# Optimization experiments

Measured on AMD Instinct MI355X. Metric: run time of the kernel, lower is better.

Reference implementation:

```python
import jax, jax.numpy as jnp
import numpy as np

DIM = 1024
HEADS = 16
DIM_HEAD = 64
INNER = HEADS * DIM_HEAD  # 1024
B, N = 2, 2048


def setup_inputs() -> dict:
    key = jax.random.key(0)
    ks = jax.random.split(key, 8)
    q = jax.random.normal(ks[0], (B, N, DIM), dtype=jnp.float32)
    k = jax.random.normal(ks[1], (B, N, DIM), dtype=jnp.float32)
    v = jax.random.normal(ks[2], (B, N, DIM), dtype=jnp.float32)
    # True = masked out (masked_fill semantics); causal mask broadcast over batch
    causal = jnp.triu(jnp.ones((N, N), dtype=jnp.bool_), k=1)
    mask = jnp.broadcast_to(causal, (B, N, N))
    s = 0.02
    Wq = jax.random.normal(ks[3], (DIM, INNER), dtype=jnp.float32) * s
    Wk = jax.random.normal(ks[4], (DIM, INNER), dtype=jnp.float32) * s
    Wv = jax.random.normal(ks[5], (DIM, INNER), dtype=jnp.float32) * s
    Wo = jax.random.normal(ks[6], (INNER, DIM), dtype=jnp.float32) * s
    bo = jnp.zeros((DIM,), dtype=jnp.float32)
    return {"q": q, "k": k, "v": v, "mask": mask,
            "Wq": Wq, "Wk": Wk, "Wv": Wv, "Wo": Wo, "bo": bo}


def reference(q, k, v, mask, Wq, Wk, Wv, Wo, bo):
    h, d = HEADS, DIM_HEAD
    scale = d ** -0.5
    b, n, _ = q.shape

    def heads_split(x):  # [b, n, h*d] -> [b, h, n, d]
        return x.reshape(b, -1, h, d).transpose(0, 2, 1, 3)

    qh = heads_split(q @ Wq)
    kh = heads_split(k @ Wk)
    vh = heads_split(v @ Wv)

    dots = jnp.einsum('bhid,bhjd->bhij', qh, kh) * scale  # [b,h,n,n]
    mask_value = -jnp.finfo(dots.dtype).max
    dots = jnp.where(mask[:, None, :, :], mask_value, dots)
    attn = jax.nn.softmax(dots, axis=-1)
    out = jnp.einsum('bhij,bhjd->bhid', attn, vh)          # [b,h,n,d]
    out = out.transpose(0, 2, 1, 3).reshape(b, n, h * d)    # [b,n,h*d]
    out = out @ Wo + bo                                     # RowParallelLinear (bias=True)
    return out  # dropout p=0.0 is identity
```

## Files before the change

### kernel.cpp

```cpp
#include <hip/hip_runtime.h>

typedef __attribute__((ext_vector_type(8))) short short8;
typedef __attribute__((ext_vector_type(4))) float f32x4;
typedef __attribute__((ext_vector_type(4))) unsigned int u32x4;

#define MFMA_BF16(a, b, c) __builtin_amdgcn_mfma_f32_16x16x32_bf16((a), (b), (c), 0, 0, 0)

#define GLOAD16(g, l) __builtin_amdgcn_global_load_lds( \
    (const __attribute__((address_space(1))) void*)(g),  \
    (__attribute__((address_space(3))) void*)(l), 16, 0, 0)

#define BARRIER() __builtin_amdgcn_s_barrier()
#define LGKMCNT0() do { asm volatile("s_waitcnt lgkmcnt(0)" ::: "memory"); \
                        __builtin_amdgcn_sched_barrier(0); } while (0)
#define VMCNT(n) asm volatile("s_waitcnt vmcnt(" n ")" ::: "memory")

static __device__ __forceinline__ unsigned short f2bf(float f) {
    unsigned int u = __builtin_bit_cast(unsigned int, f);
    u += 0x7fffu + ((u >> 16) & 1u);
    return (unsigned short)(u >> 16);
}
static __device__ __forceinline__ unsigned int cvtpk(float a, float b) {
    unsigned int r;
    asm("v_cvt_pk_bf16_f32 %0, %1, %2" : "=v"(r) : "v"(a), "v"(b));
    return r;
}
static __device__ __forceinline__ float ex2(float x) {
    float r;
    asm("v_exp_f32 %0, %1" : "=v"(r) : "v"(x));
    return r;
}

__global__ __launch_bounds__(256) void convX_kernel(
    const float* __restrict__ q, const float* __restrict__ k, const float* __restrict__ v,
    unsigned short* __restrict__ dq, unsigned short* __restrict__ dk,
    unsigned short* __restrict__ dv)
{
    const float* s; unsigned short* d;
    switch (blockIdx.y) {
        case 0:  s = q; d = dq; break;
        case 1:  s = k; d = dk; break;
        default: s = v; d = dv; break;
    }
    int i = (blockIdx.x * 256 + threadIdx.x) * 8;
    float4 a = *reinterpret_cast<const float4*>(s + i);
    float4 b = *reinterpret_cast<const float4*>(s + i + 4);
    short8 o;
    o[0] = (short)f2bf(a.x); o[1] = (short)f2bf(a.y);
    o[2] = (short)f2bf(a.z); o[3] = (short)f2bf(a.w);
    o[4] = (short)f2bf(b.x); o[5] = (short)f2bf(b.y);
    o[6] = (short)f2bf(b.z); o[7] = (short)f2bf(b.w);
    *reinterpret_cast<short8*>(d + i) = o;
}

__global__ __launch_bounds__(256) void convWT_kernel(
    const float* __restrict__ w0, const float* __restrict__ w1,
    const float* __restrict__ w2, const float* __restrict__ w3,
    unsigned short* __restrict__ t0, unsigned short* __restrict__ t1,
    unsigned short* __restrict__ t2, unsigned short* __restrict__ t3)
{
    const float* W; unsigned short* T;
    switch (blockIdx.z) {
        case 0:  W = w0; T = t0; break;
        case 1:  W = w1; T = t1; break;
        case 2:  W = w2; T = t2; break;
        default: W = w3; T = t3; break;
    }
    __shared__ unsigned short ldsT[64][72];
    const int t = threadIdx.x;
    const int kb = blockIdx.x * 64, cb = blockIdx.y * 64;

    const int c4 = (t & 15) * 4;
    const int r0 = t >> 4;
    #pragma unroll
    for (int i = 0; i < 4; ++i) {
        int kr = r0 + i * 16;
        float4 wv = *reinterpret_cast<const float4*>(&W[(size_t)(kb + kr) * 1024 + cb + c4]);
        ldsT[c4 + 0][kr] = f2bf(wv.x);
        ldsT[c4 + 1][kr] = f2bf(wv.y);
        ldsT[c4 + 2][kr] = f2bf(wv.z);
        ldsT[c4 + 3][kr] = f2bf(wv.w);
    }
    __syncthreads();
    const int c = t >> 2;
    const int kp = (t & 3) * 16;
    short8 o0 = *reinterpret_cast<const short8*>(&ldsT[c][kp]);
    short8 o1 = *reinterpret_cast<const short8*>(&ldsT[c][kp + 8]);
    *reinterpret_cast<short8*>(&T[(size_t)(cb + c) * 1024 + kb + kp])     = o0;
    *reinterpret_cast<short8*>(&T[(size_t)(cb + c) * 1024 + kb + kp + 8]) = o1;
}

__global__ __launch_bounds__(512, 2) void qkv_gemm(
    const unsigned short* __restrict__ Xq, const unsigned short* __restrict__ Xk,
    const unsigned short* __restrict__ Xv,
    const unsigned short* __restrict__ WqT, const unsigned short* __restrict__ WkT,
    const unsigned short* __restrict__ WvT,
    unsigned short* __restrict__ Qh, unsigned short* __restrict__ Kh,
    unsigned short* __restrict__ VhT)
{
    extern __shared__ unsigned short lds[];
    const int t    = threadIdx.x;
    const int lane = t & 63, w = t >> 6;
    const int lr   = lane & 15, lg = lane >> 4;
    const int wrow = w >> 2, wcol = w & 3;
    const int sw   = lr & 7;

    const int z = blockIdx.z;
    const unsigned short *A, *B; unsigned short* dst;
    int tm, cn;
    if (z == 2)      { A = WvT; B = Xv;  dst = VhT; tm = blockIdx.y * 256; cn = blockIdx.x * 256; }
    else if (z == 1) { A = Xk;  B = WkT; dst = Kh;  tm = blockIdx.x * 256; cn = blockIdx.y * 256; }
    else             { A = Xq;  B = WqT; dst = Qh;  tm = blockIdx.x * 256; cn = blockIdx.y * 256; }

    const unsigned short* Ag = A + (size_t)tm * 1024;
    const unsigned short* Bg = B + (size_t)cn * 1024;

    const int sr    = t >> 3;
    const int gsw   = (t & 7) ^ (sr & 7);
    const int brow0 = (sr >> 5) * 64 + (sr & 31);

    auto stageA = [&](int q, int kt, unsigned short* slabA) {
        const unsigned short* g = Ag + (size_t)(q * 64 + sr) * 1024 + kt + gsw * 8;
        GLOAD16(g, slabA + q * 8192 + t * 8);
        GLOAD16(g + (size_t)128 * 1024, slabA + q * 8192 + 4096 + t * 8);
    };
    auto stageB = [&](int s, int kt, unsigned short* slabB) {
        const unsigned short* g = Bg + (size_t)(brow0 + s * 32) * 1024 + kt + gsw * 8;
        GLOAD16(g, slabB + s * 8192 + t * 8);
        GLOAD16(g + (size_t)128 * 1024, slabB + s * 8192 + 4096 + t * 8);
    };

    short8 rA[4][2], rB0[2][2], rB1[2][2];
    auto ldA = [&](const unsigned short* bufA, int q) {
        #pragma unroll
        for (int m2 = 0; m2 < 4; ++m2) {
            const unsigned short* p = bufA + q * 8192 + (wrow * 64 + m2 * 16 + lr) * 64;
            rA[m2][0] = *reinterpret_cast<const short8*>(p + (lg ^ sw) * 8);
            rA[m2][1] = *reinterpret_cast<const short8*>(p + ((4 + lg) ^ sw) * 8);
        }
    };
    auto ldB = [&](const unsigned short* bufB, int s, short8 rB[2][2]) {
        #pragma unroll
        for (int n2 = 0; n2 < 2; ++n2) {
            const unsigned short* p = bufB + s * 8192 + (wcol * 32 + n2 * 16 + lr) * 64;
            rB[n2][0] = *reinterpret_cast<const short8*>(p + (lg ^ sw) * 8);
            rB[n2][1] = *reinterpret_cast<const short8*>(p + ((4 + lg) ^ sw) * 8);
        }
    };

    f32x4 acc[8][4];
    #pragma unroll
    for (int i = 0; i < 8; ++i)
        #pragma unroll
        for (int j = 0; j < 4; ++j) acc[i][j] = (f32x4){0.f, 0.f, 0.f, 0.f};

#define QUAD(MH, NH, RB) do {                                            \
    _Pragma("unroll")                                                    \
    for (int m2 = 0; m2 < 4; ++m2) {                                     \
        _Pragma("unroll")                                                \
        for (int n2 = 0; n2 < 2; ++n2) {                                 \
            f32x4 c_ = acc[(MH)*4 + m2][(NH)*2 + n2];                    \
            c_ = MFMA_BF16(rA[m2][0], (RB)[n2][0], c_);                  \
            c_ = MFMA_BF16(rA[m2][1], (RB)[n2][1], c_);                  \
            acc[(MH)*4 + m2][(NH)*2 + n2] = c_;                          \
        } } } while (0)

    stageA(0, 0, lds);
    stageB(0, 0, lds + 16384);
    stageB(1, 0, lds + 16384);
    stageA(1, 0, lds);
    VMCNT("4");
    BARRIER();

    for (int tt = 0; tt < 15; ++tt) {
        unsigned short* cA = lds + (tt & 1) * 32768;
        unsigned short* cB = cA + 16384;
        unsigned short* nA = lds + ((tt + 1) & 1) * 32768;
        unsigned short* nB = nA + 16384;
        const int kn = (tt + 1) * 64;
        stageA(0, kn, nA);
        ldA(cA, 0); ldB(cB, 0, rB0);
        VMCNT("4"); BARRIER(); LGKMCNT0();
        __builtin_amdgcn_s_setprio(1); QUAD(0, 0, rB0); __builtin_amdgcn_s_setprio(0);
        BARRIER();
        stageB(0, kn, nB);
        ldB(cB, 1, rB1);
        VMCNT("4"); BARRIER(); LGKMCNT0();
        __builtin_amdgcn_s_setprio(1); QUAD(0, 1, rB1); __builtin_amdgcn_s_setprio(0);
        BARRIER();
        stageB(1, kn, nB);
        ldA(cA, 1);
        BARRIER(); LGKMCNT0();
        __builtin_amdgcn_s_setprio(1); QUAD(1, 1, rB1); __builtin_amdgcn_s_setprio(0);
        BARRIER();
        stageA(1, kn, nA);
        VMCNT("4"); BARRIER(); LGKMCNT0();
        __builtin_amdgcn_s_setprio(1); QUAD(1, 0, rB0); __builtin_amdgcn_s_setprio(0);
        BARRIER();
    }
    {
        unsigned short* cA = lds + 32768;
        unsigned short* cB = cA + 16384;
        ldA(cA, 0); ldB(cB, 0, rB0);
        VMCNT("2"); BARRIER(); LGKMCNT0();
        __builtin_amdgcn_s_setprio(1); QUAD(0, 0, rB0); __builtin_amdgcn_s_setprio(0);
        BARRIER();
        ldB(cB, 1, rB1);
        VMCNT("0"); BARRIER(); LGKMCNT0();
        __builtin_amdgcn_s_setprio(1); QUAD(0, 1, rB1); __builtin_amdgcn_s_setprio(0);
        BARRIER();
        ldA(cA, 1);
        LGKMCNT0();
        __builtin_amdgcn_s_setprio(1); QUAD(1, 1, rB1); QUAD(1, 0, rB0);
        __builtin_amdgcn_s_setprio(0);
    }
#undef QUAD

    if (z == 2) {
        #pragma unroll
        for (int mi = 0; mi < 8; ++mi)
            #pragma unroll
            for (int ni = 0; ni < 4; ++ni)
                #pragma unroll
                for (int r = 0; r < 4; ++r) {
                    int c    = tm + wrow * 128 + mi * 16 + lg * 4 + r;
                    int nseq = cn + wcol * 64 + ni * 16 + lr;
                    int b = nseq >> 11, n = nseq & 2047;
                    int h = c >> 6, d = c & 63;
                    dst[(((size_t)(b * 16 + h) * 64 + d) << 11) + n] = f2bf(acc[mi][ni][r]);
                }
    } else {
        const float sc = (z == 0) ? 0.18033688011112042f : 1.0f;
        #pragma unroll
        for (int mi = 0; mi < 8; ++mi)
            #pragma unroll
            for (int ni = 0; ni < 4; ++ni)
                #pragma unroll
                for (int r = 0; r < 4; ++r) {
                    int orow = tm + wrow * 128 + mi * 16 + lg * 4 + r;
                    int ocol = cn + wcol * 64 + ni * 16 + lr;
                    int b = orow >> 11, n = orow & 2047;
                    int h = ocol >> 6, d = ocol & 63;
                    dst[(((size_t)(b * 16 + h) * 2048 + n) << 6) + d] = f2bf(acc[mi][ni][r] * sc);
                }
    }
}

__global__ __launch_bounds__(256) void o_gemm(
    const unsigned short* __restrict__ Ctx, const unsigned short* __restrict__ WoT,
    const float* __restrict__ bias, float* __restrict__ out)
{
    __shared__ unsigned short LB[3][8192];
    const int t = threadIdx.x;
    const int lane = t & 63, w = t >> 6;
    const int lr = lane & 15, lg = lane >> 4;
    const int wr = w >> 1, wc = w & 1;
    const int tm = blockIdx.x * 128, cn = blockIdx.y * 128;

    const int srow = w * 16 + (lane >> 2);
    const int sk   = (lane & 3) * 8;
    const unsigned short* ga = Ctx + (size_t)(tm + srow) * 1024 + sk;
    const unsigned short* gb = WoT + (size_t)(cn + srow) * 1024 + sk;
    const int lo = srow * 32 + sk;

    auto stage = [&](int k0, int bf) {
        GLOAD16(ga + k0, &LB[bf][lo]);
        GLOAD16(ga + k0 + (size_t)64 * 1024, &LB[bf][64 * 32 + lo]);
        GLOAD16(gb + k0, &LB[bf][4096 + lo]);
        GLOAD16(gb + k0 + (size_t)64 * 1024, &LB[bf][4096 + 64 * 32 + lo]);
    };

    f32x4 acc[4][4];
    #pragma unroll
    for (int i = 0; i < 4; ++i)
        #pragma unroll
        for (int j = 0; j < 4; ++j) acc[i][j] = (f32x4){0.f, 0.f, 0.f, 0.f};

    stage(0, 0);
    stage(32, 1);

    int cur = 0;
    for (int s = 0; s < 32; ++s) {
        if (s + 1 < 32) { VMCNT("4"); } else { VMCNT("0"); }
        BARRIER();
        __builtin_amdgcn_sched_barrier(0);
        if (s + 2 < 32) {
            int nb = cur + 2; if (nb >= 3) nb -= 3;
            stage(32 * (s + 2), nb);
        }

        short8 af[4], bfr[4];
        #pragma unroll
        for (int i = 0; i < 4; ++i) {
            af[i]  = *reinterpret_cast<const short8*>(&LB[cur][(wr * 64 + i * 16 + lr) * 32 + lg * 8]);
            bfr[i] = *reinterpret_cast<const short8*>(&LB[cur][4096 + (wc * 64 + i * 16 + lr) * 32 + lg * 8]);
        }
        __builtin_amdgcn_s_setprio(1);
        #pragma unroll
        for (int mi = 0; mi < 4; ++mi)
            #pragma unroll
            for (int ni = 0; ni < 4; ++ni)
                acc[mi][ni] = MFMA_BF16(af[mi], bfr[ni], acc[mi][ni]);
        __builtin_amdgcn_s_setprio(0);

        cur = (cur + 1 == 3) ? 0 : cur + 1;
    }

    #pragma unroll
    for (int mi = 0; mi < 4; ++mi)
        #pragma unroll
        for (int ni = 0; ni < 4; ++ni)
            #pragma unroll
            for (int r = 0; r < 4; ++r) {
                int orow = tm + wr * 64 + mi * 16 + lg * 4 + r;
                int ocol = cn + wc * 64 + ni * 16 + lr;
                out[(size_t)orow * 1024 + ocol] = acc[mi][ni][r] + bias[ocol];
            }
}

__global__ __launch_bounds__(256, 2) void attn_kernel(
    const unsigned short* __restrict__ Qh, const unsigned short* __restrict__ Kh,
    const unsigned short* __restrict__ VhT, unsigned short* __restrict__ Ctx)
{
    __shared__ unsigned short KV[3][8192];

    const int t  = threadIdx.x;
    const int l  = t & 63, w = t >> 6;
    const int lr = l & 15, lg = l >> 4;
    const int rg = w & 1, jh = w >> 1;
    const int swz = lr & 7;

    const int lin  = blockIdx.x;
    const int xcd  = lin & 7;
    const int j    = lin >> 3;
    const int bh   = xcd * 4 + (j & 3);
    const int u    = j >> 2;
    const int strip = (u & 1) ? (u >> 1) : (31 - (u >> 1));
    const int b    = bh >> 4, h = bh & 15;

    const unsigned short* Qb = Qh  + (size_t)bh * (2048 * 64);
    const unsigned short* Kb = Kh  + (size_t)bh * (2048 * 64);
    const unsigned short* Vb = VhT + (size_t)bh * (64 * 2048);

    const int srow = t >> 3;
    const int sg   = (t & 7) ^ (srow & 7);

    auto stage = [&](int jt, int bf) {
        const unsigned short* kg0 = Kb + (size_t)(jt + srow) * 64 + sg * 8;
        unsigned short* kl = &KV[bf][0] + w * 512;
        GLOAD16(kg0, kl);
        GLOAD16(kg0 + 32 * 64, kl + 2048);
        const unsigned short* vg0 = Vb + (size_t)srow * 2048 + jt + sg * 8;
        unsigned short* vl = &KV[bf][4096] + w * 512;
        GLOAD16(vg0, vl);
        GLOAD16(vg0 + (size_t)32 * 2048, vl + 2048);
    };

    const int qbase = strip * 64 + rg * 32;
    const int ns    = strip + 1;

    short8 bQ[2][2];
    #pragma unroll
    for (int qg = 0; qg < 2; ++qg) {
        const unsigned short* qp = Qb + (size_t)(qbase + qg * 16 + lr) * 64 + lg * 8;
        bQ[qg][0] = *reinterpret_cast<const short8*>(qp);
        bQ[qg][1] = *reinterpret_cast<const short8*>(qp + 32);
    }

    f32x4 acc[2][4];
    #pragma unroll
    for (int qg = 0; qg < 2; ++qg)
        #pragma unroll
        for (int di = 0; di < 4; ++di) acc[qg][di] = (f32x4){0.f, 0.f, 0.f, 0.f};
    float lsum[2] = {0.f, 0.f};

    stage(0, 0);
    if (ns > 1) stage(64, 1);

    int cur = 0;
    for (int s = 0; s < ns; ++s) {
        if (s + 1 < ns) { VMCNT("4"); } else { VMCNT("0"); }
        BARRIER();
        __builtin_amdgcn_sched_barrier(0);
        if (s + 2 < ns) {
            int nb = cur + 2; if (nb >= 3) nb -= 3;
            stage(64 * (s + 2), nb);
        }

        const int jt = 64 * s + jh * 32;
        const unsigned short* Ks = &KV[cur][0];
        const unsigned short* Vs = &KV[cur][4096];

        short8 aK[2][2];
        #pragma unroll
        for (int kg = 0; kg < 2; ++kg) {
            const int rT = jh * 32 + kg * 16 + lr;
            aK[kg][0] = *reinterpret_cast<const short8*>(Ks + rT * 64 + ((lg ^ swz) << 3));
            aK[kg][1] = *reinterpret_cast<const short8*>(Ks + rT * 64 + (((4 + lg) ^ swz) << 3));
        }
        short8 bV[4];
        #pragma unroll
        for (int di = 0; di < 4; ++di) {
            const int d = lr + 16 * di;
            bV[di] = *reinterpret_cast<const short8*>(Vs + d * 64 + (((jh * 4 + lg) ^ swz) << 3));
        }

        f32x4 sf[2][2];
        __builtin_amdgcn_s_setprio(1);
        #pragma unroll
        for (int kg = 0; kg < 2; ++kg)
            #pragma unroll
            for (int qg = 0; qg < 2; ++qg) {
                f32x4 z = (f32x4){0.f, 0.f, 0.f, 0.f};
                z = MFMA_BF16(aK[kg][0], bQ[qg][0], z);
                sf[kg][qg] = MFMA_BF16(aK[kg][1], bQ[qg][1], z);
            }
        __builtin_amdgcn_s_setprio(0);

        #pragma unroll
        for (int qg = 0; qg < 2; ++qg) {
            const int qrow = qbase + qg * 16 + lr;
            float p[8];
            if (jt + 31 > qbase + qg * 16) {
                #pragma unroll
                for (int r = 0; r < 4; ++r) {
                    p[r]     = (jt + lg * 4 + r      > qrow) ? 0.f : ex2(sf[0][qg][r]);
                    p[4 + r] = (jt + 16 + lg * 4 + r > qrow) ? 0.f : ex2(sf[1][qg][r]);
                }
            } else {
                #pragma unroll
                for (int r = 0; r < 4; ++r) {
                    p[r] = ex2(sf[0][qg][r]); p[4 + r] = ex2(sf[1][qg][r]);
                }
            }

            lsum[qg] += (p[0] + p[1]) + (p[2] + p[3]) + (p[4] + p[5]) + (p[6] + p[7]);

            unsigned int c0 = cvtpk(p[0], p[1]);
            unsigned int c1 = cvtpk(p[2], p[3]);
            unsigned int c2 = cvtpk(p[4], p[5]);
            unsigned int c3 = cvtpk(p[6], p[7]);
            asm("v_permlane32_swap_b32 %0, %1" : "+v"(c0), "+v"(c2));
            asm("v_permlane32_swap_b32 %0, %1" : "+v"(c1), "+v"(c3));
            asm("v_permlane16_swap_b32 %0, %1" : "+v"(c0), "+v"(c2));
            asm("v_permlane16_swap_b32 %0, %1" : "+v"(c1), "+v"(c3));
            short8 aP = __builtin_bit_cast(short8, (u32x4){c0, c1, c2, c3});

            __builtin_amdgcn_s_setprio(1);
            #pragma unroll
            for (int di = 0; di < 4; ++di)
                acc[qg][di] = MFMA_BF16(aP, bV[di], acc[qg][di]);
            __builtin_amdgcn_s_setprio(0);
        }

        cur = (cur + 1 == 3) ? 0 : cur + 1;
    }

    #pragma unroll
    for (int qg = 0; qg < 2; ++qg) {
        lsum[qg] += __shfl_xor(lsum[qg], 16);
        lsum[qg] += __shfl_xor(lsum[qg], 32);
    }

    __syncthreads();

    float* cmb = (float*)&KV[0][0];
    if (jh == 1) {
        float* cp = cmb + (size_t)(rg * 64 + l) * 36;
        #pragma unroll
        for (int qg = 0; qg < 2; ++qg)
            #pragma unroll
            for (int di = 0; di < 4; ++di)
                *reinterpret_cast<f32x4*>(cp + (qg * 4 + di) * 4) = acc[qg][di];
        cp[32] = lsum[0]; cp[33] = lsum[1];
    }
    __syncthreads();
    if (jh == 0) {
        const float* cp = cmb + (size_t)(rg * 64 + l) * 36;
        #pragma unroll
        for (int qg = 0; qg < 2; ++qg) {
            #pragma unroll
            for (int di = 0; di < 4; ++di)
                acc[qg][di] += *reinterpret_cast<const f32x4*>(cp + (qg * 4 + di) * 4);
            float lt = lsum[qg] + cp[32 + qg];
            float linv[4];
            #pragma unroll
            for (int r = 0; r < 4; ++r) linv[r] = 1.f / __shfl(lt, lg * 4 + r);
            #pragma unroll
            for (int di = 0; di < 4; ++di) {
                #pragma unroll
                for (int r = 0; r < 4; ++r) {
                    int row = qbase + qg * 16 + lg * 4 + r;
                    Ctx[(size_t)(b * 2048 + row) * 1024 + h * 64 + di * 16 + lr] =
                        f2bf(acc[qg][di][r] * linv[r]);
                }
            }
        }
    }
}

extern "C" void kernel_launch(void* const* d_in, const int* in_sizes, int n_in,
                              void* d_out, int out_size, void* d_ws, size_t ws_size,
                              hipStream_t stream) {
    const float* q  = (const float*)d_in[0];
    const float* k  = (const float*)d_in[1];
    const float* v  = (const float*)d_in[2];
    const float* Wq = (const float*)d_in[4];
    const float* Wk = (const float*)d_in[5];
    const float* Wv = (const float*)d_in[6];
    const float* Wo = (const float*)d_in[7];
    const float* bo = (const float*)d_in[8];
    float* out = (float*)d_out;

    const size_t HSZ = (size_t)32 * 2048 * 64;
    const size_t WSZ = (size_t)1024 * 1024;
    unsigned short* Qh  = (unsigned short*)d_ws;
    unsigned short* Kh  = Qh + HSZ;
    unsigned short* VhT = Kh + HSZ;
    unsigned short* Xqb = VhT + HSZ;
    unsigned short* Xkb = Xqb + HSZ;
    unsigned short* Xvb = Xkb + HSZ;
    unsigned short* WqT = Xvb + HSZ;
    unsigned short* WkT = WqT + WSZ;
    unsigned short* WvT = WkT + WSZ;
    unsigned short* WoT = WvT + WSZ;
    unsigned short* Ctx = Xqb;

    hipFuncSetAttribute(reinterpret_cast<const void*>(qkv_gemm),
                        hipFuncAttributeMaxDynamicSharedMemorySize, 131072);

    dim3 blk(256);
    convX_kernel<<<dim3(2048, 3), blk, 0, stream>>>(q, k, v, Xqb, Xkb, Xvb);
    convWT_kernel<<<dim3(16, 16, 4), blk, 0, stream>>>(Wq, Wk, Wv, Wo, WqT, WkT, WvT, WoT);
    qkv_gemm<<<dim3(16, 4, 3), dim3(512), 131072, stream>>>(Xqb, Xkb, Xvb, WqT, WkT, WvT, Qh, Kh, VhT);
    attn_kernel<<<dim3(1024), blk, 0, stream>>>(Qh, Kh, VhT, Ctx);
    o_gemm<<<dim3(32, 8), blk, 0, stream>>>(Ctx, WoT, bo, out);
}
```

Measured before the change: 102.0 us.

## Load V fragments directly to registers and fuse conversion kernels

The attention kernel now stages only K through LDS. Each lane loads its V fragments straight from global memory into registers, double-buffered one step ahead, which halves the LDS footprint and lets launch bounds ask for 5 blocks per CU instead of 2. The two fp32-to-bf16 conversion kernels are merged into one launch, saving a kernel launch. The direct V loads use small strided accesses that may coalesce poorly, and the extra register buffer raises register pressure under the tighter occupancy target.

```diff
diff --git a/kernel.cpp b/kernel.cpp
--- a/kernel.cpp
+++ b/kernel.cpp
@@ -31,44 +31,49 @@
     return r;
 }
 
-__global__ __launch_bounds__(256) void convX_kernel(
+__global__ __launch_bounds__(256) void conv_all(
     const float* __restrict__ q, const float* __restrict__ k, const float* __restrict__ v,
     unsigned short* __restrict__ dq, unsigned short* __restrict__ dk,
-    unsigned short* __restrict__ dv)
-{
-    const float* s; unsigned short* d;
-    switch (blockIdx.y) {
-        case 0:  s = q; d = dq; break;
-        case 1:  s = k; d = dk; break;
-        default: s = v; d = dv; break;
-    }
-    int i = (blockIdx.x * 256 + threadIdx.x) * 8;
-    float4 a = *reinterpret_cast<const float4*>(s + i);
-    float4 b = *reinterpret_cast<const float4*>(s + i + 4);
-    short8 o;
-    o[0] = (short)f2bf(a.x); o[1] = (short)f2bf(a.y);
-    o[2] = (short)f2bf(a.z); o[3] = (short)f2bf(a.w);
-    o[4] = (short)f2bf(b.x); o[5] = (short)f2bf(b.y);
-    o[6] = (short)f2bf(b.z); o[7] = (short)f2bf(b.w);
-    *reinterpret_cast<short8*>(d + i) = o;
-}
-
-__global__ __launch_bounds__(256) void convWT_kernel(
+    unsigned short* __restrict__ dv,
     const float* __restrict__ w0, const float* __restrict__ w1,
     const float* __restrict__ w2, const float* __restrict__ w3,
     unsigned short* __restrict__ t0, unsigned short* __restrict__ t1,
     unsigned short* __restrict__ t2, unsigned short* __restrict__ t3)
 {
+    __shared__ unsigned short ldsT[64][72];
+    const int idx = blockIdx.x;
+    const int t = threadIdx.x;
+
+    if (idx < 6144) {
+        const int bx = idx & 2047, by = idx >> 11;
+        const float* s; unsigned short* d;
+        switch (by) {
+            case 0:  s = q; d = dq; break;
+            case 1:  s = k; d = dk; break;
+            default: s = v; d = dv; break;
+        }
+        int i = (bx * 256 + t) * 8;
+        float4 a = *reinterpret_cast<const float4*>(s + i);
+        float4 b = *reinterpret_cast<const float4*>(s + i + 4);
+        short8 o;
+        o[0] = (short)f2bf(a.x); o[1] = (short)f2bf(a.y);
+        o[2] = (short)f2bf(a.z); o[3] = (short)f2bf(a.w);
+        o[4] = (short)f2bf(b.x); o[5] = (short)f2bf(b.y);
+        o[6] = (short)f2bf(b.z); o[7] = (short)f2bf(b.w);
+        *reinterpret_cast<short8*>(d + i) = o;
+        return;
+    }
+
+    const int zi = idx - 6144;
+    const int bx = zi & 15, by = (zi >> 4) & 15, bz = zi >> 8;
     const float* W; unsigned short* T;
-    switch (blockIdx.z) {
+    switch (bz) {
         case 0:  W = w0; T = t0; break;
         case 1:  W = w1; T = t1; break;
         case 2:  W = w2; T = t2; break;
         default: W = w3; T = t3; break;
     }
-    __shared__ unsigned short ldsT[64][72];
-    const int t = threadIdx.x;
-    const int kb = blockIdx.x * 64, cb = blockIdx.y * 64;
+    const int kb = bx * 64, cb = by * 64;
 
     const int c4 = (t & 15) * 4;
     const int r0 = t >> 4;
@@ -318,11 +323,11 @@
             }
 }
 
-__global__ __launch_bounds__(256, 2) void attn_kernel(
+__global__ __launch_bounds__(256, 5) void attn_kernel(
     const unsigned short* __restrict__ Qh, const unsigned short* __restrict__ Kh,
     const unsigned short* __restrict__ VhT, unsigned short* __restrict__ Ctx)
 {
-    __shared__ unsigned short KV[3][8192];
+    __shared__ unsigned short KL[3][4096];
 
     const int t  = threadIdx.x;
     const int l  = t & 63, w = t >> 6;
@@ -345,20 +350,32 @@
     const int srow = t >> 3;
     const int sg   = (t & 7) ^ (srow & 7);
 
-    auto stage = [&](int jt, int bf) {
+    auto stageK = [&](int jt, int bf) {
         const unsigned short* kg0 = Kb + (size_t)(jt + srow) * 64 + sg * 8;
-        unsigned short* kl = &KV[bf][0] + w * 512;
+        unsigned short* kl = &KL[bf][0] + w * 512;
         GLOAD16(kg0, kl);
         GLOAD16(kg0 + 32 * 64, kl + 2048);
-        const unsigned short* vg0 = Vb + (size_t)srow * 2048 + jt + sg * 8;
-        unsigned short* vl = &KV[bf][4096] + w * 512;
-        GLOAD16(vg0, vl);
-        GLOAD16(vg0 + (size_t)32 * 2048, vl + 2048);
+    };
+    const unsigned short* vpb = Vb + (size_t)lr * 2048 + lg * 8;
+    auto loadV = [&](int jt, short8 bV[4]) {
+        #pragma unroll
+        for (int di = 0; di < 4; ++di)
+            bV[di] = *reinterpret_cast<const short8*>(vpb + (size_t)(16 * di) * 2048 + jt);
     };
 
     const int qbase = strip * 64 + rg * 32;
     const int ns    = strip + 1;
 
+    f32x4 acc[2][4];
+    #pragma unroll
+    for (int qg = 0; qg < 2; ++qg)
+        #pragma unroll
+        for (int di = 0; di < 4; ++di) acc[qg][di] = (f32x4){0.f, 0.f, 0.f, 0.f};
+    float lsum[2] = {0.f, 0.f};
+
+    stageK(0, 0);
+    short8 bV[4], bVn[4];
+    loadV(jh * 32, bV);
     short8 bQ[2][2];
     #pragma unroll
     for (int qg = 0; qg < 2; ++qg) {
@@ -366,30 +383,21 @@
         bQ[qg][0] = *reinterpret_cast<const short8*>(qp);
         bQ[qg][1] = *reinterpret_cast<const short8*>(qp + 32);
     }
-
-    f32x4 acc[2][4];
-    #pragma unroll
-    for (int qg = 0; qg < 2; ++qg)
-        #pragma unroll
-        for (int di = 0; di < 4; ++di) acc[qg][di] = (f32x4){0.f, 0.f, 0.f, 0.f};
-    float lsum[2] = {0.f, 0.f};
-
-    stage(0, 0);
-    if (ns > 1) stage(64, 1);
+    if (ns > 1) stageK(64, 1);
 
     int cur = 0;
     for (int s = 0; s < ns; ++s) {
-        if (s + 1 < ns) { VMCNT("4"); } else { VMCNT("0"); }
+        if (s + 1 < ns) { VMCNT("2"); } else { VMCNT("0"); }
         BARRIER();
         __builtin_amdgcn_sched_barrier(0);
+        if (s + 1 < ns) loadV(64 * (s + 1) + jh * 32, bVn);
         if (s + 2 < ns) {
             int nb = cur + 2; if (nb >= 3) nb -= 3;
-            stage(64 * (s + 2), nb);
+            stageK(64 * (s + 2), nb);
         }
 
         const int jt = 64 * s + jh * 32;
-        const unsigned short* Ks = &KV[cur][0];
-        const unsigned short* Vs = &KV[cur][4096];
+        const unsigned short* Ks = &KL[cur][0];
 
         short8 aK[2][2];
         #pragma unroll
@@ -397,12 +405,6 @@
             const int rT = jh * 32 + kg * 16 + lr;
             aK[kg][0] = *reinterpret_cast<const short8*>(Ks + rT * 64 + ((lg ^ swz) << 3));
             aK[kg][1] = *reinterpret_cast<const short8*>(Ks + rT * 64 + (((4 + lg) ^ swz) << 3));
-        }
-        short8 bV[4];
-        #pragma unroll
-        for (int di = 0; di < 4; ++di) {
-            const int d = lr + 16 * di;
-            bV[di] = *reinterpret_cast<const short8*>(Vs + d * 64 + (((jh * 4 + lg) ^ swz) << 3));
         }
 
         f32x4 sf[2][2];
@@ -453,6 +455,8 @@
             __builtin_amdgcn_s_setprio(0);
         }
 
+        #pragma unroll
+        for (int di = 0; di < 4; ++di) bV[di] = bVn[di];
         cur = (cur + 1 == 3) ? 0 : cur + 1;
     }
 
@@ -464,7 +468,7 @@
 
     __syncthreads();
 
-    float* cmb = (float*)&KV[0][0];
+    float* cmb = (float*)&KL[0][0];
     if (jh == 1) {
         float* cp = cmb + (size_t)(rg * 64 + l) * 36;
         #pragma unroll
@@ -530,8 +534,8 @@
                         hipFuncAttributeMaxDynamicSharedMemorySize, 131072);
 
     dim3 blk(256);
-    convX_kernel<<<dim3(2048, 3), blk, 0, stream>>>(q, k, v, Xqb, Xkb, Xvb);
-    convWT_kernel<<<dim3(16, 16, 4), blk, 0, stream>>>(Wq, Wk, Wv, Wo, WqT, WkT, WvT, WoT);
+    conv_all<<<dim3(7168), blk, 0, stream>>>(q, k, v, Xqb, Xkb, Xvb,
+                                             Wq, Wk, Wv, Wo, WqT, WkT, WvT, WoT);
     qkv_gemm<<<dim3(16, 4, 3), dim3(512), 131072, stream>>>(Xqb, Xkb, Xvb, WqT, WkT, WvT, Qh, Kh, VhT);
     attn_kernel<<<dim3(1024), blk, 0, stream>>>(Qh, Kh, VhT, Ctx);
     o_gemm<<<dim3(32, 8), blk, 0, stream>>>(Ctx, WoT, bo, out);
```

New measurement: 323.4 us. 217% more time.
